# Kernel tuning notes

Hardware: AMD Instinct MI355X
Metric: run time of the kernel (lower is better)

The kernel has to match this reference:

```python
import jax, jax.numpy as jnp
import numpy as np
from jax import lax

KERNEL = 5  # cv2 np.ones((5,5)) structuring element
EDGE_WEIGHT = 0.1


def _edge_weights(target):
    # target: [B,1,H,W] float. Binary mask -> morphological gradient via
    # max-pool (dilate) and min-pool (erode) with 5x5 window, SAME padding.
    # cv2 pads dilate with -inf and erode with +inf, so padding never
    # creates or removes foreground; reduce_window init values match that.
    b = (target > 0.5).astype(target.dtype)
    win = (1, 1, KERNEL, KERNEL)
    ones = (1, 1, 1, 1)
    dilated = lax.reduce_window(b, jnp.float32(-jnp.inf), lax.max, win, ones, 'SAME')
    eroded = lax.reduce_window(b, jnp.float32(jnp.inf), lax.min, win, ones, 'SAME')
    edge = dilated - eroded
    # Samples with empty masks get edge==0 everywhere, so the per-sample
    # binary_mask.sum()>0 guard in the original is a no-op here.
    return jnp.where(edge > 0, jnp.float32(EDGE_WEIGHT), jnp.float32(1.0))


def setup_inputs() -> dict:
    key = jax.random.key(0)
    k1, k2 = jax.random.split(key)
    shape = (32, 1, 1024, 1024)
    pred = jax.random.normal(k1, shape, dtype=jnp.float32)
    target = jax.random.randint(k2, shape, 0, 2).astype(jnp.float32)
    return {"pred": pred, "target": target}


def reference(pred, target):
    # BCEWithLogitsLoss(reduction='none'): softplus(x) - x*t (stable form)
    loss = jax.nn.softplus(pred) - pred * target
    # Weighting branch only taken when target.max()==1 and target.min()==0
    cond = jnp.logical_and(target.max() == 1.0, target.min() == 0.0)
    weights = _edge_weights(target)
    weights = jnp.where(cond, weights, jnp.float32(1.0))
    return (loss * weights).mean()
```

## Files before the change

### kernel.cpp

```cpp
#include <hip/hip_runtime.h>


#define IMG   1024
#define BAND  32
#define NB    32
#define WORDS 16
#define NTOT  33554432.0

__device__ __forceinline__ unsigned encf(float f) {
    unsigned u = __float_as_uint(f);
    return (u & 0x80000000u) ? ~u : (u | 0x80000000u);
}
__device__ __forceinline__ float decf(unsigned e) {
    unsigned u = (e & 0x80000000u) ? (e & 0x7fffffffu) : ~e;
    return __uint_as_float(u);
}

__global__ void bbl_init(double* dws, unsigned* uws) {
    if (threadIdx.x == 0) {
        dws[0] = 0.0; dws[1] = 0.0;
        uws[0] = 0xFFFFFFFFu;
        uws[1] = 0u;
    }
}

__global__ __launch_bounds__(256) void bbl_main(
        const float* __restrict__ pred,
        const float* __restrict__ target,
        double* __restrict__ dws, unsigned* __restrict__ uws) {
    __shared__ unsigned long long Bm[BAND + 4][WORDS];
    __shared__ unsigned long long H1[BAND + 4][WORDS];
    __shared__ unsigned long long H0[BAND + 4][WORDS];
    __shared__ unsigned long long Em[BAND][WORDS];
    __shared__ float    redS1[4], redSe[4];
    __shared__ unsigned redMn[4], redMx[4];

    const int tid  = threadIdx.x;
    const int lane = tid & 63;
    const int wid  = tid >> 6;
    const int img  = blockIdx.x / (IMG / BAND);
    const int r0   = (blockIdx.x % (IMG / BAND)) * BAND;
    const int hs   = max(r0 - 2, 0);
    const int he   = min(r0 + BAND + 2, IMG);
    const int nLoaded = he - hs;

    const size_t imgBase = (size_t)img * IMG * IMG;

    float vmin = 3.4e38f, vmax = -3.4e38f;

    for (int lr = wid; lr < nLoaded; lr += 4) {
        const int gr = hs + lr;
        const float* rowp = target + imgBase + (size_t)gr * IMG;
        #pragma unroll
        for (int it = 0; it < WORDS; ++it) {
            float v = rowp[it * 64 + lane];
            vmin = fminf(vmin, v); vmax = fmaxf(vmax, v);
            unsigned long long m = __ballot(v > 0.5f);
            if (lane == 0) Bm[lr][it] = m;
        }
    }
    __syncthreads();

    for (int q = tid; q < nLoaded * WORDS; q += 256) {
        const int lr = q >> 4, w = q & 15;
        unsigned long long c = Bm[lr][w];
        unsigned long long l = (w > 0)         ? Bm[lr][w - 1] : 0ULL;
        unsigned long long r = (w < WORDS - 1) ? Bm[lr][w + 1] : 0ULL;
        unsigned long long h1 = c | (c << 1) | (l >> 63) | (c << 2) | (l >> 62)
                                  | (c >> 1) | (r << 63) | (c >> 2) | (r << 62);
        unsigned long long n  = ~c;
        unsigned long long nl = (w > 0)         ? ~l : 0ULL;
        unsigned long long nr = (w < WORDS - 1) ? ~r : 0ULL;
        unsigned long long h0 = n | (n << 1) | (nl >> 63) | (n << 2) | (nl >> 62)
                                  | (n >> 1) | (nr << 63) | (n >> 2) | (nr << 62);
        H1[lr][w] = h1; H0[lr][w] = h0;
    }
    __syncthreads();

    for (int q = tid; q < BAND * WORDS; q += 256) {
        const int orow = q >> 4, w = q & 15;
        const int gr = r0 + orow;
        const int lo = max(gr - 2, 0), hi = min(gr + 2, IMG - 1);
        unsigned long long a1 = 0ULL, a0 = 0ULL;
        for (int g = lo; g <= hi; ++g) { a1 |= H1[g - hs][w]; a0 |= H0[g - hs][w]; }
        Em[orow][w] = a1 & a0;
    }
    __syncthreads();

    float s1 = 0.f, se = 0.f;
    for (int orow = wid; orow < BAND; orow += 4) {
        const int gr = r0 + orow;
        const int lr = gr - hs;
        const float4* rowp = (const float4*)(pred + imgBase + (size_t)gr * IMG);
        #pragma unroll
        for (int it = 0; it < 4; ++it) {
            float4 p4 = rowp[it * 64 + lane];
            const int wi = it * 4 + (lane >> 4);
            const int sh = (lane & 15) * 4;
            unsigned eb = (unsigned)((Em[orow][wi] >> sh) & 0xFULL);
            unsigned tb = (unsigned)((Bm[lr][wi]  >> sh) & 0xFULL);
            float p[4] = {p4.x, p4.y, p4.z, p4.w};
            #pragma unroll
            for (int k = 0; k < 4; ++k) {
                float x = p[k];
                float t = (float)((tb >> k) & 1u);
                float loss = fmaxf(x, 0.f) + __logf(1.f + __expf(-fabsf(x))) - x * t;
                s1 += loss;
                se += ((eb >> k) & 1u) ? loss : 0.f;
            }
        }
    }

    for (int off = 32; off > 0; off >>= 1) {
        s1  += __shfl_down(s1, off);
        se  += __shfl_down(se, off);
        vmin = fminf(vmin, __shfl_down(vmin, off));
        vmax = fmaxf(vmax, __shfl_down(vmax, off));
    }
    if (lane == 0) {
        redS1[wid] = s1; redSe[wid] = se;
        redMn[wid] = encf(vmin); redMx[wid] = encf(vmax);
    }
    __syncthreads();
    if (tid == 0) {
        float S1 = 0.f, Se = 0.f; unsigned mn = 0xFFFFFFFFu, mx = 0u;
        for (int i = 0; i < 4; ++i) {
            S1 += redS1[i]; Se += redSe[i];
            mn = min(mn, redMn[i]); mx = max(mx, redMx[i]);
        }
        atomicAdd(&dws[0], (double)S1);
        atomicAdd(&dws[1], (double)Se);
        atomicMin(&uws[0], mn);
        atomicMax(&uws[1], mx);
    }
}

__global__ void bbl_fin(const double* __restrict__ dws,
                        const unsigned* __restrict__ uws,
                        float* __restrict__ out) {
    if (threadIdx.x == 0) {
        float fmin = decf(uws[0]);
        float fmax = decf(uws[1]);
        bool cond = (fmax == 1.0f) && (fmin == 0.0f);
        double s = cond ? (dws[0] - 0.9 * dws[1]) : dws[0];
        out[0] = (float)(s / NTOT);
    }
}

extern "C" void kernel_launch(void* const* d_in, const int* in_sizes, int n_in,
                              void* d_out, int out_size, void* d_ws, size_t ws_size,
                              hipStream_t stream) {
    const float* pred   = (const float*)d_in[0];
    const float* target = (const float*)d_in[1];
    double*   dws = (double*)d_ws;
    unsigned* uws = (unsigned*)(dws + 2);
    float*    out = (float*)d_out;

    hipLaunchKernelGGL(bbl_init, dim3(1), dim3(64), 0, stream, dws, uws);
    hipLaunchKernelGGL(bbl_main, dim3(NB * (IMG / BAND)), dim3(256), 0, stream,
                       pred, target, dws, uws);
    hipLaunchKernelGGL(bbl_fin, dim3(1), dim3(64), 0, stream, dws, uws, out);
}
```

Before: 356.1 us.

## Vectorize target loads, use strided bit layout, separable vertical-first morphology, 512 threads

Target rows are now read as float4, and four ballots pack each lane's components into interleaved bitmask words. This turns the per-row load into fewer, wider transactions. The morphology now runs vertical-first (OR/AND over five rows), then horizontal using the strided bit layout with cross-word carries, and it drops the separate H1/H0 passes. Blocks grow to 512 threads with one thread per output word. The horizontal neighbor indexing is more intricate and carries a risk of edge-case bugs.

```diff
diff --git a/kernel.cpp b/kernel.cpp
--- a/kernel.cpp
+++ b/kernel.cpp
@@ -1,11 +1,16 @@
 #include <hip/hip_runtime.h>
 
 
-#define IMG   1024
-#define BAND  32
-#define NB    32
-#define WORDS 16
-#define NTOT  33554432.0
+#define IMG     1024
+#define BAND    32
+#define NBANDS  (IMG / BAND)
+#define NIMG    32
+#define WORDS   16
+#define HALO    2
+#define MAXROWS (BAND + 2 * HALO)
+#define NTOT    33554432.0
+
+typedef unsigned long long u64;
 
 __device__ __forceinline__ unsigned encf(float f) {
     unsigned u = __float_as_uint(f);
@@ -24,98 +29,121 @@
     }
 }
 
-__global__ __launch_bounds__(256) void bbl_main(
+__global__ __launch_bounds__(512) void bbl_main(
         const float* __restrict__ pred,
         const float* __restrict__ target,
         double* __restrict__ dws, unsigned* __restrict__ uws) {
-    __shared__ unsigned long long Bm[BAND + 4][WORDS];
-    __shared__ unsigned long long H1[BAND + 4][WORDS];
-    __shared__ unsigned long long H0[BAND + 4][WORDS];
-    __shared__ unsigned long long Em[BAND][WORDS];
-    __shared__ float    redS1[4], redSe[4];
-    __shared__ unsigned redMn[4], redMx[4];
+    __shared__ u64 Bm[MAXROWS][WORDS];
+    __shared__ u64 Vd[BAND][WORDS];
+    __shared__ u64 Ve[BAND][WORDS];
+    __shared__ u64 Em[BAND][WORDS];
+    __shared__ float    redS1[8], redSe[8];
+    __shared__ unsigned redMn[8], redMx[8];
 
     const int tid  = threadIdx.x;
     const int lane = tid & 63;
     const int wid  = tid >> 6;
-    const int img  = blockIdx.x / (IMG / BAND);
-    const int r0   = (blockIdx.x % (IMG / BAND)) * BAND;
-    const int hs   = max(r0 - 2, 0);
-    const int he   = min(r0 + BAND + 2, IMG);
+    const int img  = blockIdx.x / NBANDS;
+    const int r0   = (blockIdx.x % NBANDS) * BAND;
+    const int hs   = max(r0 - HALO, 0);
+    const int he   = min(r0 + BAND + HALO, IMG);
     const int nLoaded = he - hs;
-
-    const size_t imgBase = (size_t)img * IMG * IMG;
+    const size_t base = (size_t)img * IMG * IMG;
 
     float vmin = 3.4e38f, vmax = -3.4e38f;
 
-    for (int lr = wid; lr < nLoaded; lr += 4) {
-        const int gr = hs + lr;
-        const float* rowp = target + imgBase + (size_t)gr * IMG;
+    for (int lr = wid; lr < nLoaded; lr += 8) {
+        const float4* rowp = (const float4*)(target + base + (size_t)(hs + lr) * IMG);
         #pragma unroll
-        for (int it = 0; it < WORDS; ++it) {
-            float v = rowp[it * 64 + lane];
-            vmin = fminf(vmin, v); vmax = fmaxf(vmax, v);
-            unsigned long long m = __ballot(v > 0.5f);
-            if (lane == 0) Bm[lr][it] = m;
+        for (int it = 0; it < 4; ++it) {
+            float4 v = rowp[it * 64 + lane];
+            vmin = fminf(vmin, fminf(fminf(v.x, v.y), fminf(v.z, v.w)));
+            vmax = fmaxf(vmax, fmaxf(fmaxf(v.x, v.y), fmaxf(v.z, v.w)));
+            u64 b0 = __ballot(v.x > 0.5f);
+            u64 b1 = __ballot(v.y > 0.5f);
+            u64 b2 = __ballot(v.z > 0.5f);
+            u64 b3 = __ballot(v.w > 0.5f);
+            if (lane < 4) {
+                u64 w = (lane == 0) ? b0 : (lane == 1) ? b1 : (lane == 2) ? b2 : b3;
+                Bm[lr][it * 4 + lane] = w;
+            }
         }
     }
     __syncthreads();
 
-    for (int q = tid; q < nLoaded * WORDS; q += 256) {
-        const int lr = q >> 4, w = q & 15;
-        unsigned long long c = Bm[lr][w];
-        unsigned long long l = (w > 0)         ? Bm[lr][w - 1] : 0ULL;
-        unsigned long long r = (w < WORDS - 1) ? Bm[lr][w + 1] : 0ULL;
-        unsigned long long h1 = c | (c << 1) | (l >> 63) | (c << 2) | (l >> 62)
-                                  | (c >> 1) | (r << 63) | (c >> 2) | (r << 62);
-        unsigned long long n  = ~c;
-        unsigned long long nl = (w > 0)         ? ~l : 0ULL;
-        unsigned long long nr = (w < WORDS - 1) ? ~r : 0ULL;
-        unsigned long long h0 = n | (n << 1) | (nl >> 63) | (n << 2) | (nl >> 62)
-                                  | (n >> 1) | (nr << 63) | (n >> 2) | (nr << 62);
-        H1[lr][w] = h1; H0[lr][w] = h0;
+    {
+        const int orow = tid >> 4, w = tid & 15;
+        const int gr = r0 + orow;
+        const int lo = max(gr - 2, 0), hi = min(gr + 2, IMG - 1);
+        u64 vd = 0ULL, ve = ~0ULL;
+        for (int g = lo; g <= hi; ++g) { u64 b = Bm[g - hs][w]; vd |= b; ve &= b; }
+        Vd[orow][w] = vd; Ve[orow][w] = ve;
     }
     __syncthreads();
 
-    for (int q = tid; q < BAND * WORDS; q += 256) {
-        const int orow = q >> 4, w = q & 15;
-        const int gr = r0 + orow;
-        const int lo = max(gr - 2, 0), hi = min(gr + 2, IMG - 1);
-        unsigned long long a1 = 0ULL, a0 = 0ULL;
-        for (int g = lo; g <= hi; ++g) { a1 |= H1[g - hs][w]; a0 |= H0[g - hs][w]; }
-        Em[orow][w] = a1 & a0;
+    {
+        const int orow = tid >> 4, w = tid & 15;
+        const int k = w & 3;
+        u64 hd = Vd[orow][w], he_ = Ve[orow][w];
+        #pragma unroll
+        for (int dd = 0; dd < 4; ++dd) {
+            const int delta = (dd < 2) ? dd - 2 : dd - 1;
+            const int kp = k + delta;
+            u64 td, te;
+            if (kp >= 0 && kp <= 3) {
+                td = Vd[orow][w + delta];
+                te = Ve[orow][w + delta];
+            } else if (kp > 3) {
+                const int wi = w + delta - 4, wn = w + delta;
+                u64 nd = (wn <= 15) ? Vd[orow][wn] : 0ULL;
+                u64 ne = (wn <= 15) ? Ve[orow][wn] : ~0ULL;
+                td = (Vd[orow][wi] >> 1) | (nd << 63);
+                te = (Ve[orow][wi] >> 1) | (ne << 63);
+            } else {
+                const int wi = w + delta + 4, wn = w + delta;
+                u64 nd = (wn >= 0) ? Vd[orow][wn] : 0ULL;
+                u64 ne = (wn >= 0) ? Ve[orow][wn] : ~0ULL;
+                td = (Vd[orow][wi] << 1) | (nd >> 63);
+                te = (Ve[orow][wi] << 1) | (ne >> 63);
+            }
+            hd |= td; he_ &= te;
+        }
+        Em[orow][w] = hd & ~he_;
     }
     __syncthreads();
 
     float s1 = 0.f, se = 0.f;
-    for (int orow = wid; orow < BAND; orow += 4) {
-        const int gr = r0 + orow;
-        const int lr = gr - hs;
-        const float4* rowp = (const float4*)(pred + imgBase + (size_t)gr * IMG);
+    for (int orow = wid * 4; orow < wid * 4 + 4; ++orow) {
+        const int gr = r0 + orow, lr = gr - hs;
+        const float4* rowp = (const float4*)(pred + base + (size_t)gr * IMG);
         #pragma unroll
         for (int it = 0; it < 4; ++it) {
-            float4 p4 = rowp[it * 64 + lane];
-            const int wi = it * 4 + (lane >> 4);
-            const int sh = (lane & 15) * 4;
-            unsigned eb = (unsigned)((Em[orow][wi] >> sh) & 0xFULL);
-            unsigned tb = (unsigned)((Bm[lr][wi]  >> sh) & 0xFULL);
-            float p[4] = {p4.x, p4.y, p4.z, p4.w};
-            #pragma unroll
-            for (int k = 0; k < 4; ++k) {
-                float x = p[k];
-                float t = (float)((tb >> k) & 1u);
-                float loss = fmaxf(x, 0.f) + __logf(1.f + __expf(-fabsf(x))) - x * t;
-                s1 += loss;
-                se += ((eb >> k) & 1u) ? loss : 0.f;
-            }
+            float4 p = rowp[it * 64 + lane];
+            u64 e0 = Em[orow][it * 4 + 0], e1 = Em[orow][it * 4 + 1];
+            u64 e2 = Em[orow][it * 4 + 2], e3 = Em[orow][it * 4 + 3];
+            u64 t0 = Bm[lr][it * 4 + 0],   t1 = Bm[lr][it * 4 + 1];
+            u64 t2 = Bm[lr][it * 4 + 2],   t3 = Bm[lr][it * 4 + 3];
+            float x, t, loss;
+            x = p.x; t = (float)((unsigned)((t0 >> lane) & 1ULL));
+            loss = fmaxf(x, 0.f) - x * t + __logf(1.f + __expf(-fabsf(x)));
+            s1 += loss; se += ((e0 >> lane) & 1ULL) ? loss : 0.f;
+            x = p.y; t = (float)((unsigned)((t1 >> lane) & 1ULL));
+            loss = fmaxf(x, 0.f) - x * t + __logf(1.f + __expf(-fabsf(x)));
+            s1 += loss; se += ((e1 >> lane) & 1ULL) ? loss : 0.f;
+            x = p.z; t = (float)((unsigned)((t2 >> lane) & 1ULL));
+            loss = fmaxf(x, 0.f) - x * t + __logf(1.f + __expf(-fabsf(x)));
+            s1 += loss; se += ((e2 >> lane) & 1ULL) ? loss : 0.f;
+            x = p.w; t = (float)((unsigned)((t3 >> lane) & 1ULL));
+            loss = fmaxf(x, 0.f) - x * t + __logf(1.f + __expf(-fabsf(x)));
+            s1 += loss; se += ((e3 >> lane) & 1ULL) ? loss : 0.f;
         }
     }
 
     for (int off = 32; off > 0; off >>= 1) {
-        s1  += __shfl_down(s1, off);
-        se  += __shfl_down(se, off);
-        vmin = fminf(vmin, __shfl_down(vmin, off));
-        vmax = fmaxf(vmax, __shfl_down(vmax, off));
+        s1   += __shfl_down(s1, off);
+        se   += __shfl_down(se, off);
+        vmin  = fminf(vmin, __shfl_down(vmin, off));
+        vmax  = fmaxf(vmax, __shfl_down(vmax, off));
     }
     if (lane == 0) {
         redS1[wid] = s1; redSe[wid] = se;
@@ -124,7 +152,8 @@
     __syncthreads();
     if (tid == 0) {
         float S1 = 0.f, Se = 0.f; unsigned mn = 0xFFFFFFFFu, mx = 0u;
-        for (int i = 0; i < 4; ++i) {
+        #pragma unroll
+        for (int i = 0; i < 8; ++i) {
             S1 += redS1[i]; Se += redSe[i];
             mn = min(mn, redMn[i]); mx = max(mx, redMx[i]);
         }
@@ -157,7 +186,7 @@
     float*    out = (float*)d_out;
 
     hipLaunchKernelGGL(bbl_init, dim3(1), dim3(64), 0, stream, dws, uws);
-    hipLaunchKernelGGL(bbl_main, dim3(NB * (IMG / BAND)), dim3(256), 0, stream,
+    hipLaunchKernelGGL(bbl_main, dim3(NIMG * NBANDS), dim3(512), 0, stream,
                        pred, target, dws, uws);
     hipLaunchKernelGGL(bbl_fin, dim3(1), dim3(64), 0, stream, dws, uws, out);
 }
```

Result: faster. 296.6 us (-16.7%).

## Compute morphology per wavefront in registers with a rolling 5-row bitmask window

Applied to the files above, without the earlier changes.

Each wavefront now owns 8 rows of one image and keeps a sliding window of five row bitmasks in registers. Vertical dilate/erode are done with OR/AND over the window, and horizontal ones with cross-lane 64-bit shuffles. This replaces the shared-memory bitmask, H1/H0 and Em staging and the block barriers. Target rows are loaded as float4, but the two halo rows on each side are re-read per 8-row wavefront, so redundant target reads rise compared with the 32-row bands. Per-element mask bits are fetched with readlane broadcasts, which adds scalar work inside the hot loop.

```diff
diff --git a/kernel.cpp b/kernel.cpp
--- a/kernel.cpp
+++ b/kernel.cpp
@@ -1,11 +1,22 @@
 #include <hip/hip_runtime.h>
 
 
-#define IMG   1024
-#define BAND  32
-#define NB    32
-#define WORDS 16
-#define NTOT  33554432.0
+#define IMG  1024
+#define RPW  8
+#define NTOT 33554432.0
+
+typedef unsigned long long u64;
+
+__device__ __forceinline__ u64 shfl64(u64 v, int src) {
+    unsigned lo = (unsigned)__shfl((int)(unsigned)(v & 0xffffffffULL), src, 64);
+    unsigned hi = (unsigned)__shfl((int)(unsigned)(v >> 32), src, 64);
+    return ((u64)hi << 32) | lo;
+}
+__device__ __forceinline__ u64 bcast64(u64 v, int srcImm) {
+    unsigned lo = (unsigned)__builtin_amdgcn_readlane((int)(unsigned)(v & 0xffffffffULL), srcImm);
+    unsigned hi = (unsigned)__builtin_amdgcn_readlane((int)(unsigned)(v >> 32), srcImm);
+    return ((u64)hi << 32) | lo;
+}
 
 __device__ __forceinline__ unsigned encf(float f) {
     unsigned u = __float_as_uint(f);
@@ -28,94 +39,120 @@
         const float* __restrict__ pred,
         const float* __restrict__ target,
         double* __restrict__ dws, unsigned* __restrict__ uws) {
-    __shared__ unsigned long long Bm[BAND + 4][WORDS];
-    __shared__ unsigned long long H1[BAND + 4][WORDS];
-    __shared__ unsigned long long H0[BAND + 4][WORDS];
-    __shared__ unsigned long long Em[BAND][WORDS];
     __shared__ float    redS1[4], redSe[4];
     __shared__ unsigned redMn[4], redMx[4];
 
     const int tid  = threadIdx.x;
     const int lane = tid & 63;
     const int wid  = tid >> 6;
-    const int img  = blockIdx.x / (IMG / BAND);
-    const int r0   = (blockIdx.x % (IMG / BAND)) * BAND;
-    const int hs   = max(r0 - 2, 0);
-    const int he   = min(r0 + BAND + 2, IMG);
-    const int nLoaded = he - hs;
-
-    const size_t imgBase = (size_t)img * IMG * IMG;
+    const int gw   = blockIdx.x * 4 + wid;
+    const int img  = gw >> 7;
+    const int r0   = (gw & 127) * RPW;
+    const size_t base = (size_t)img * IMG * IMG;
+    const float* tbase = target + base;
+    const float* pbase = pred + base;
+
+    const int w = lane & 15;
+    const int k = w & 3;
 
     float vmin = 3.4e38f, vmax = -3.4e38f;
-
-    for (int lr = wid; lr < nLoaded; lr += 4) {
-        const int gr = hs + lr;
-        const float* rowp = target + imgBase + (size_t)gr * IMG;
-        #pragma unroll
-        for (int it = 0; it < WORDS; ++it) {
-            float v = rowp[it * 64 + lane];
-            vmin = fminf(vmin, v); vmax = fmaxf(vmax, v);
-            unsigned long long m = __ballot(v > 0.5f);
-            if (lane == 0) Bm[lr][it] = m;
-        }
-    }
-    __syncthreads();
-
-    for (int q = tid; q < nLoaded * WORDS; q += 256) {
-        const int lr = q >> 4, w = q & 15;
-        unsigned long long c = Bm[lr][w];
-        unsigned long long l = (w > 0)         ? Bm[lr][w - 1] : 0ULL;
-        unsigned long long r = (w < WORDS - 1) ? Bm[lr][w + 1] : 0ULL;
-        unsigned long long h1 = c | (c << 1) | (l >> 63) | (c << 2) | (l >> 62)
-                                  | (c >> 1) | (r << 63) | (c >> 2) | (r << 62);
-        unsigned long long n  = ~c;
-        unsigned long long nl = (w > 0)         ? ~l : 0ULL;
-        unsigned long long nr = (w < WORDS - 1) ? ~r : 0ULL;
-        unsigned long long h0 = n | (n << 1) | (nl >> 63) | (n << 2) | (nl >> 62)
-                                  | (n >> 1) | (nr << 63) | (n >> 2) | (nr << 62);
-        H1[lr][w] = h1; H0[lr][w] = h0;
-    }
-    __syncthreads();
-
-    for (int q = tid; q < BAND * WORDS; q += 256) {
-        const int orow = q >> 4, w = q & 15;
-        const int gr = r0 + orow;
-        const int lo = max(gr - 2, 0), hi = min(gr + 2, IMG - 1);
-        unsigned long long a1 = 0ULL, a0 = 0ULL;
-        for (int g = lo; g <= hi; ++g) { a1 |= H1[g - hs][w]; a0 |= H0[g - hs][w]; }
-        Em[orow][w] = a1 & a0;
-    }
-    __syncthreads();
-
     float s1 = 0.f, se = 0.f;
-    for (int orow = wid; orow < BAND; orow += 4) {
-        const int gr = r0 + orow;
-        const int lr = gr - hs;
-        const float4* rowp = (const float4*)(pred + imgBase + (size_t)gr * IMG);
+
+    auto loadrow = [&](int gr, bool mm) -> u64 {
+        const float4* rp = (const float4*)(tbase + (size_t)gr * IMG);
+        u64 myw = 0ULL;
         #pragma unroll
         for (int it = 0; it < 4; ++it) {
-            float4 p4 = rowp[it * 64 + lane];
-            const int wi = it * 4 + (lane >> 4);
-            const int sh = (lane & 15) * 4;
-            unsigned eb = (unsigned)((Em[orow][wi] >> sh) & 0xFULL);
-            unsigned tb = (unsigned)((Bm[lr][wi]  >> sh) & 0xFULL);
-            float p[4] = {p4.x, p4.y, p4.z, p4.w};
+            float4 v = rp[it * 64 + lane];
+            if (mm) {
+                vmin = fminf(vmin, fminf(fminf(v.x, v.y), fminf(v.z, v.w)));
+                vmax = fmaxf(vmax, fmaxf(fmaxf(v.x, v.y), fmaxf(v.z, v.w)));
+            }
+            u64 b0 = __ballot(v.x > 0.5f);
+            u64 b1 = __ballot(v.y > 0.5f);
+            u64 b2 = __ballot(v.z > 0.5f);
+            u64 b3 = __ballot(v.w > 0.5f);
+            u64 bw = (k == 0) ? b0 : (k == 1) ? b1 : (k == 2) ? b2 : b3;
+            if ((w >> 2) == it) myw = bw;
+        }
+        return myw;
+    };
+
+    u64 q0 = loadrow(max(r0 - 2, 0), false);
+    u64 q1 = loadrow(max(r0 - 1, 0), false);
+    u64 q2 = loadrow(r0, true);
+    u64 q3 = loadrow(r0 + 1, true);
+
+    for (int r = r0; r < r0 + RPW; ++r) {
+        const int nr = min(r + 2, IMG - 1);
+        u64 q4 = loadrow(nr, r + 2 <= r0 + RPW - 1);
+
+        const float4* pp = (const float4*)(pbase + (size_t)r * IMG);
+        float4 p0 = pp[0 * 64 + lane];
+        float4 p1 = pp[1 * 64 + lane];
+        float4 p2 = pp[2 * 64 + lane];
+        float4 p3 = pp[3 * 64 + lane];
+
+        u64 vd = q0 | q1 | q2 | q3 | q4;
+        u64 ve = q0 & q1 & q2 & q3 & q4;
+        u64 ct = q2;
+
+        u64 hd = vd, he = ve;
+        #pragma unroll
+        for (int di = 0; di < 4; ++di) {
+            const int d = (di < 2) ? di - 2 : di - 1;
+            int wp = w + d;
+            bool inp = (wp >= 0) && (wp < 16);
+            u64 ad = shfl64(vd, wp & 15);
+            u64 ae = shfl64(ve, wp & 15);
+            ad = inp ? ad : 0ULL;
+            ae = inp ? ae : ~0ULL;
+            int ws2 = wp + ((d > 0) ? -4 : 4);
+            u64 bd = shfl64(vd, ws2 & 15);
+            u64 be = shfl64(ve, ws2 & 15);
+            int kp = k + d;
+            u64 rd, re;
+            if (d > 0) {
+                u64 wd = (bd >> 1) | (ad << 63);
+                u64 we = (be >> 1) | (ae << 63);
+                rd = (kp <= 3) ? ad : wd;
+                re = (kp <= 3) ? ae : we;
+            } else {
+                u64 wd = (bd << 1) | (ad >> 63);
+                u64 we = (be << 1) | (ae >> 63);
+                rd = (kp >= 0) ? ad : wd;
+                re = (kp >= 0) ? ae : we;
+            }
+            hd |= rd; he &= re;
+        }
+        u64 em = hd & ~he;
+
+        #pragma unroll
+        for (int it = 0; it < 4; ++it) {
+            float4 p = (it == 0) ? p0 : (it == 1) ? p1 : (it == 2) ? p2 : p3;
             #pragma unroll
-            for (int k = 0; k < 4; ++k) {
-                float x = p[k];
-                float t = (float)((tb >> k) & 1u);
-                float loss = fmaxf(x, 0.f) + __logf(1.f + __expf(-fabsf(x))) - x * t;
+            for (int m = 0; m < 4; ++m) {
+                u64 ew = bcast64(em, it * 4 + m);
+                u64 tw = bcast64(ct, it * 4 + m);
+                float x = (m == 0) ? p.x : (m == 1) ? p.y : (m == 2) ? p.z : p.w;
+                unsigned tb = (unsigned)(tw >> lane) & 1u;
+                unsigned eb = (unsigned)(ew >> lane) & 1u;
+                float xt = tb ? x : 0.f;
+                float sp = fmaxf(x, 0.f) + __logf(1.f + __expf(-fabsf(x)));
+                float loss = sp - xt;
                 s1 += loss;
-                se += ((eb >> k) & 1u) ? loss : 0.f;
+                se += eb ? loss : 0.f;
             }
         }
+
+        q0 = q1; q1 = q2; q2 = q3; q3 = q4;
     }
 
     for (int off = 32; off > 0; off >>= 1) {
-        s1  += __shfl_down(s1, off);
-        se  += __shfl_down(se, off);
-        vmin = fminf(vmin, __shfl_down(vmin, off));
-        vmax = fmaxf(vmax, __shfl_down(vmax, off));
+        s1   += __shfl_down(s1, off);
+        se   += __shfl_down(se, off);
+        vmin  = fminf(vmin, __shfl_down(vmin, off));
+        vmax  = fmaxf(vmax, __shfl_down(vmax, off));
     }
     if (lane == 0) {
         redS1[wid] = s1; redSe[wid] = se;
@@ -124,6 +161,7 @@
     __syncthreads();
     if (tid == 0) {
         float S1 = 0.f, Se = 0.f; unsigned mn = 0xFFFFFFFFu, mx = 0u;
+        #pragma unroll
         for (int i = 0; i < 4; ++i) {
             S1 += redS1[i]; Se += redSe[i];
             mn = min(mn, redMn[i]); mx = max(mx, redMx[i]);
@@ -157,7 +195,7 @@
     float*    out = (float*)d_out;
 
     hipLaunchKernelGGL(bbl_init, dim3(1), dim3(64), 0, stream, dws, uws);
-    hipLaunchKernelGGL(bbl_main, dim3(NB * (IMG / BAND)), dim3(256), 0, stream,
+    hipLaunchKernelGGL(bbl_main, dim3(1024), dim3(256), 0, stream,
                        pred, target, dws, uws);
     hipLaunchKernelGGL(bbl_fin, dim3(1), dim3(64), 0, stream, dws, uws, out);
 }
```

Result: faster. 313.0 us (-12.1%).
